# Kernel tuning notes

Measured on AMD Instinct MI355X. Metric: run time of the kernel, lower is better.

Reference implementation:

```python
import jax, jax.numpy as jnp
import numpy as np

ANCHORS_ALL = jnp.array([[10.,13.],[16.,30.],[33.,23.],[30.,61.],[62.,45.],
                         [59.,119.],[116.,90.],[156.,198.],[373.,326.]], dtype=jnp.float32)
INDICES = jnp.array([0, 1, 2], dtype=jnp.int32)   # anchor indices of level 0
ANCH_LVL = ANCHORS_ALL[0:3]                        # [nA, 2] anchors for this level
STRIDE = 8.0
N_CLS = 80
NA = 3


def _bce_logits(x, t):
    # elementwise binary_cross_entropy_with_logits (same formula as torch)
    return jnp.maximum(x, 0.0) - x * t + jnp.log1p(jnp.exp(-jnp.abs(x)))


def _iou_cxcywh(a, b):
    # a: [..., 4], b: [..., 4] (broadcastable), boxes as (cx, cy, w, h)
    ax1, ax2 = a[..., 0] - a[..., 2] * 0.5, a[..., 0] + a[..., 2] * 0.5
    ay1, ay2 = a[..., 1] - a[..., 3] * 0.5, a[..., 1] + a[..., 3] * 0.5
    bx1, bx2 = b[..., 0] - b[..., 2] * 0.5, b[..., 0] + b[..., 2] * 0.5
    by1, by2 = b[..., 1] - b[..., 3] * 0.5, b[..., 1] + b[..., 3] * 0.5
    iw = jnp.clip(jnp.minimum(ax2, bx2) - jnp.maximum(ax1, bx1), 0.0)
    ih = jnp.clip(jnp.minimum(ay2, by2) - jnp.maximum(ay1, by1), 0.0)
    inter = iw * ih
    union = (ax2 - ax1) * (ay2 - ay1) + (bx2 - bx1) * (by2 - by1) - inter
    return inter / (union + 1e-16)


def setup_inputs() -> dict:
    key = jax.random.key(0)
    ks = jax.random.split(key, 7)
    nB, nA, nH, nW, G = 8, 3, 160, 160, 32
    t_bbox = jax.random.normal(ks[0], (nB, nA, nH, nW, 4), jnp.float32)
    conf_logits = jax.random.normal(ks[1], (nB, nA, nH, nW, 1), jnp.float32)
    cls_logits = jax.random.normal(ks[2], (nB, nA, nH, nW, N_CLS), jnp.float32)
    cxy = jax.random.uniform(ks[3], (nB, G, 2), jnp.float32, 20.0, 1260.0)
    wh = jax.random.uniform(ks[4], (nB, G, 2), jnp.float32, 5.0, 60.0)
    gt_bboxes = jnp.concatenate([cxy, wh], axis=-1)           # cxcywh
    gt_cls = jax.random.randint(ks[5], (nB, G), 0, N_CLS, jnp.int32)
    gt_mask = jax.random.uniform(ks[6], (nB, G)) < 0.8        # padded-GT validity
    return dict(t_bbox=t_bbox, conf_logits=conf_logits, cls_logits=cls_logits,
                gt_bboxes=gt_bboxes, gt_cls=gt_cls, gt_mask=gt_mask)


def reference(t_bbox, conf_logits, cls_logits, gt_bboxes, gt_cls, gt_mask):
    nB, nA, nH, nW, _ = t_bbox.shape
    N = nA * nH * nW
    # ---- bbox decode (torch does this on a detached copy) ----
    sig = jax.nn.sigmoid(jax.lax.stop_gradient(t_bbox))
    yv, xv = jnp.meshgrid(jnp.arange(nH), jnp.arange(nW), indexing='ij')
    grid = jnp.stack([xv, yv], axis=-1).astype(jnp.float32).reshape(1, 1, nH, nW, 2)
    p_xy = (sig[..., 0:2] * 2.0 - 0.5 + grid) * STRIDE
    p_wh = (sig[..., 2:4] * 2.0) ** 2 * ANCH_LVL.reshape(1, nA, 1, 1, 2)
    p_bbox = jnp.concatenate([p_xy, p_wh], axis=-1).reshape(nB, N, 4)
    p_conf = jax.nn.sigmoid(jax.lax.stop_gradient(conf_logits))       # [nB,nA,nH,nW,1]
    p_cls = jax.nn.sigmoid(jax.lax.stop_gradient(cls_logits))
    cls_score = jnp.max(p_cls, axis=-1, keepdims=True)
    cls_idx = jnp.argmax(p_cls, axis=-1).reshape(nB, N)
    score = (p_conf * cls_score).reshape(nB, N)
    # ---- per-GT best-anchor matching (vectorized over [nB, G]) ----
    gw, gh = gt_bboxes[..., 2], gt_bboxes[..., 3]
    aw, ah = ANCHORS_ALL[:, 0], ANCHORS_ALL[:, 1]
    inter = jnp.minimum(gw[..., None], aw) * jnp.minimum(gh[..., None], ah)
    union = (gw * gh)[..., None] + aw * ah - inter
    anch_idx = jnp.argmax(inter / (union + 1e-16), axis=-1)           # [nB,G]
    matched = jnp.any(anch_idx[..., None] == INDICES, axis=-1)
    valid = gt_mask & matched
    ta = (anch_idx % NA).astype(jnp.int32)
    ti = jnp.clip((gt_bboxes[..., 0] / STRIDE).astype(jnp.int32), 0, nW - 1)
    tj = jnp.clip((gt_bboxes[..., 1] / STRIDE).astype(jnp.int32), 0, nH - 1)
    b_idx = jnp.arange(nB)[:, None]
    t_bb = t_bbox[b_idx, ta, tj, ti]       # [nB,G,4]
    t_cl = cls_logits[b_idx, ta, tj, ti]   # [nB,G,C]
    tgt_xy = ((gt_bboxes[..., 0:2] / STRIDE) % 1.0 + 0.5) / 2.0
    tgt_wh = jnp.sqrt(gt_bboxes[..., 2:4] / ANCH_LVL[ta]) / 2.0
    vm = valid.astype(t_bbox.dtype)
    loss_xy = jnp.sum(vm * jnp.sum(_bce_logits(t_bb[..., 0:2], tgt_xy), axis=-1))
    loss_wh = jnp.sum(vm * jnp.sum(_bce_logits(t_bb[..., 2:4], tgt_wh), axis=-1))
    onehot = jax.nn.one_hot(gt_cls, N_CLS, dtype=t_bbox.dtype)
    loss_cls = jnp.sum(vm * jnp.mean(_bce_logits(t_cl, onehot), axis=-1))
    # ---- objectness target: max IoU of every decoded box with the GTs ----
    ious = _iou_cxcywh(p_bbox[:, :, None, :], gt_bboxes[:, None, :, :])  # [nB,N,G]
    ious = jnp.where(gt_mask[:, None, :], ious, -1.0)
    has_gt = jnp.any(gt_mask, axis=-1)
    tconf = jnp.where(has_gt[:, None], jnp.max(ious, axis=-1), 0.0)
    tconf = tconf.reshape(nB, nA, nH, nW, 1)
    loss_conf = jnp.sum(_bce_logits(conf_logits, tconf))
    loss = (loss_xy + loss_wh + loss_conf + loss_cls) / nB
    return p_bbox, cls_idx, score, loss
```

## Files before the change

kernel.cpp:

```cpp
#include <hip/hip_runtime.h>

#define NB 8
#define NA 3
#define NH 160
#define NW 160
#define NCLS 80
#define NGT 32
#define NPB (NA * NH * NW)
#define TOTAL (NB * NPB)
#define NBLK (TOTAL / 256)
#define OFF_CLSIDX (TOTAL * 4)
#define OFF_SCORE  (TOTAL * 5)
#define OFF_LOSS   (TOTAL * 6)

#define F4_PER_ROW 20

__device__ float g_acc = 0.0f;

__device__ __forceinline__ float det_sigmoid(float x) { return 1.0f / (1.0f + expf(-x)); }
__device__ __forceinline__ float det_bce(float x, float t) {
    return fmaxf(x, 0.0f) - x * t + log1pf(expf(-fabsf(x)));
}
__device__ __forceinline__ float det_aw3(int a) { return a == 0 ? 10.0f : (a == 1 ? 16.0f : 33.0f); }
__device__ __forceinline__ float det_ah3(int a) { return a == 0 ? 13.0f : (a == 1 ? 30.0f : 23.0f); }

__device__ __forceinline__ bool det_mask_is_u8(const void* p) {
    const unsigned int* w = (const unsigned int*)p;
    unsigned int acc = 0;
#pragma unroll
    for (int k = 0; k < 64; k++) acc |= (w[k] & 0xFFFFFF00u);
    return acc != 0;
}
__device__ __forceinline__ bool det_mask_at(const void* p, bool u8mode, int idx) {
    return u8mode ? (((const unsigned char*)p)[idx] != 0)
                  : (((const int*)p)[idx] != 0);
}

__device__ __forceinline__ float det_gt_loss(int tid,
        const float* __restrict__ t_bbox,
        const float* __restrict__ cls_logits,
        const float* __restrict__ gt_bboxes,
        const int* __restrict__ gt_cls,
        const void* __restrict__ gt_mask) {
    bool u8mode = det_mask_is_u8(gt_mask);
    int b = tid >> 5;
    int g = tid & 31;
    float4 gtb = ((const float4*)gt_bboxes)[b * NGT + g];
    float cx = gtb.x, cy = gtb.y, gw = gtb.z, gh = gtb.w;

    const float aw9[9] = {10.f,16.f,33.f,30.f,62.f,59.f,116.f,156.f,373.f};
    const float ah9[9] = {13.f,30.f,23.f,61.f,45.f,119.f,90.f,198.f,326.f};
    float garea = gw * gh;
    int aidx = 0;
    float best = -1.0f;
#pragma unroll
    for (int k = 0; k < 9; k++) {
        float inter = fminf(gw, aw9[k]) * fminf(gh, ah9[k]);
        float uni = garea + aw9[k] * ah9[k] - inter;
        float r = inter / (uni + 1e-16f);
        if (r > best) { best = r; aidx = k; }
    }
    bool valid = det_mask_at(gt_mask, u8mode, b * NGT + g) && (aidx < NA);
    int ta = aidx % NA;
    int ti = min(max((int)(cx * 0.125f), 0), NW - 1);
    int tj = min(max((int)(cy * 0.125f), 0), NH - 1);
    size_t cell = ((size_t)(b * NA + ta) * NH + tj) * NW + ti;

    float4 tb = ((const float4*)t_bbox)[cell];
    float fx = cx * 0.125f; fx -= floorf(fx);
    float fy = cy * 0.125f; fy -= floorf(fy);
    float tx = (fx + 0.5f) * 0.5f;
    float ty = (fy + 0.5f) * 0.5f;
    float tw = sqrtf(gw / det_aw3(ta)) * 0.5f;
    float th = sqrtf(gh / det_ah3(ta)) * 0.5f;

    float l = det_bce(tb.x, tx) + det_bce(tb.y, ty) +
              det_bce(tb.z, tw) + det_bce(tb.w, th);

    const float4* cl = (const float4*)(cls_logits + cell * NCLS);
    int tc = gt_cls[b * NGT + g];
    float lc = 0.0f;
#pragma unroll
    for (int c4 = 0; c4 < NCLS / 4; c4++) {
        float4 v = cl[c4];
        int c = c4 * 4;
        lc += det_bce(v.x, (c + 0 == tc) ? 1.0f : 0.0f);
        lc += det_bce(v.y, (c + 1 == tc) ? 1.0f : 0.0f);
        lc += det_bce(v.z, (c + 2 == tc) ? 1.0f : 0.0f);
        lc += det_bce(v.w, (c + 3 == tc) ? 1.0f : 0.0f);
    }
    l += lc * (1.0f / NCLS);
    return valid ? l : 0.0f;
}

__device__ __forceinline__ void det_issue_tile(const float4* g4, float4* ldsbase,
                                               size_t f4base, int l) {
#pragma unroll
    for (int k = 0; k < 5; ++k) {
        __builtin_amdgcn_global_load_lds(
            (const __attribute__((address_space(1))) void*)(g4 + f4base + k * 64 + l),
            (__attribute__((address_space(3))) void*)(ldsbase + k * 64),
            16, 0, 0);
    }
}

#define DET_WAITVM0() do { \
    asm volatile("s_waitcnt vmcnt(0)" ::: "memory"); \
    __builtin_amdgcn_sched_barrier(0); \
} while (0)
#define DET_WAITLGKM0() do { \
    asm volatile("s_waitcnt lgkmcnt(0)" ::: "memory"); \
    __builtin_amdgcn_sched_barrier(0); \
} while (0)

__global__ __launch_bounds__(256, 7) void det_all_k(
    const float* __restrict__ t_bbox,
    const float* __restrict__ conf_logits,
    const float* __restrict__ cls_logits,
    const float* __restrict__ gt_bboxes,
    const int* __restrict__ gt_cls,
    const void* __restrict__ gt_mask,
    float* __restrict__ out) {
    __shared__ float4 s_cls[4][16 * F4_PER_ROW];
    __shared__ float4 s_box[NGT];
    __shared__ float2 s_am[NGT];
    __shared__ float s_part[4];

    int tid = threadIdx.x;
    int blockCell = blockIdx.x * 256;
    int gid = blockCell + tid;
    int b = gid / NPB;
    int r = gid % NPB;

    if (tid < NGT) {
        bool u8mode = det_mask_is_u8(gt_mask);
        float4 gtb = ((const float4*)gt_bboxes)[b * NGT + tid];
        float4 bx;
        bx.x = gtb.x - gtb.z * 0.5f;
        bx.y = gtb.y - gtb.w * 0.5f;
        bx.z = gtb.x + gtb.z * 0.5f;
        bx.w = gtb.y + gtb.w * 0.5f;
        s_box[tid] = bx;
        float2 am;
        am.x = gtb.z * gtb.w;
        am.y = det_mask_at(gt_mask, u8mode, b * NGT + tid) ? 1.0f : 0.0f;
        s_am[tid] = am;
    }
    __syncthreads();

    int a   = r / (NH * NW);
    int rem = r % (NH * NW);
    int j   = rem / NW;
    int i   = rem % NW;

    float4 tb = ((const float4*)t_bbox)[gid];
    float confl = conf_logits[gid];
    float s0 = det_sigmoid(tb.x), s1 = det_sigmoid(tb.y);
    float s2 = det_sigmoid(tb.z), s3 = det_sigmoid(tb.w);
    float px = (s0 * 2.0f - 0.5f + (float)i) * 8.0f;
    float py = (s1 * 2.0f - 0.5f + (float)j) * 8.0f;
    float sw = s2 * 2.0f, sh = s3 * 2.0f;
    float pw = sw * sw * det_aw3(a);
    float ph = sh * sh * det_ah3(a);
    float4 pb; pb.x = px; pb.y = py; pb.z = pw; pb.w = ph;
    ((float4*)out)[gid] = pb;

    int w = tid >> 6, l = tid & 63;
    int cl_ = l >> 2;
    int q   = l & 3;
    const float4* g4 = (const float4*)cls_logits;
    int wbase = blockCell + w * 64;
    float4* t0 = &s_cls[w][0];
    __builtin_amdgcn_sched_barrier(0);
    det_issue_tile(g4, t0, (size_t)wbase * F4_PER_ROW, l);
    __builtin_amdgcn_sched_barrier(0);

    float px1 = px - pw * 0.5f, px2 = px + pw * 0.5f;
    float py1 = py - ph * 0.5f, py2 = py + ph * 0.5f;
    float parea = pw * ph;
    float maxiou = 0.0f;
#pragma unroll
    for (int g = 0; g < NGT; g++) {
        float4 bx = s_box[g];
        float2 am = s_am[g];
        float iw = fmaxf(fminf(px2, bx.z) - fmaxf(px1, bx.x), 0.0f);
        float ih = fmaxf(fminf(py2, bx.w) - fmaxf(py1, bx.y), 0.0f);
        float inter = iw * ih;
        float uni = parea + am.x - inter;
        float iou = inter / (uni + 1e-16f);
        maxiou = fmaxf(maxiou, (am.y != 0.0f) ? iou : 0.0f);
    }

    float sconf = det_sigmoid(confl);
    float lconf = det_bce(confl, maxiou);

    if (blockIdx.x == 0)
        lconf += det_gt_loss(tid, t_bbox, cls_logits, gt_bboxes, gt_cls, gt_mask);

#pragma unroll
    for (int off = 32; off > 0; off >>= 1) lconf += __shfl_down(lconf, off, 64);
    if (l == 0) s_part[w] = lconf;

#pragma unroll
    for (int it = 0; it < 4; ++it) {
        DET_WAITVM0();
        const float4* rowp = t0 + cl_ * F4_PER_ROW + q * 5;
        float4 v0 = rowp[0];
        float4 v1 = rowp[1];
        float4 v2 = rowp[2];
        float4 v3 = rowp[3];
        float4 v4 = rowp[4];
        DET_WAITLGKM0();
        if (it < 3)
            det_issue_tile(g4, t0, (size_t)(wbase + (it + 1) * 16) * F4_PER_ROW, l);

        float mx = -1e30f;
        int mi = 0;
        int cb = q * 20;
        { int c = cb;
          if (v0.x > mx) { mx = v0.x; mi = c + 0; }
          if (v0.y > mx) { mx = v0.y; mi = c + 1; }
          if (v0.z > mx) { mx = v0.z; mi = c + 2; }
          if (v0.w > mx) { mx = v0.w; mi = c + 3; } }
        { int c = cb + 4;
          if (v1.x > mx) { mx = v1.x; mi = c + 0; }
          if (v1.y > mx) { mx = v1.y; mi = c + 1; }
          if (v1.z > mx) { mx = v1.z; mi = c + 2; }
          if (v1.w > mx) { mx = v1.w; mi = c + 3; } }
        { int c = cb + 8;
          if (v2.x > mx) { mx = v2.x; mi = c + 0; }
          if (v2.y > mx) { mx = v2.y; mi = c + 1; }
          if (v2.z > mx) { mx = v2.z; mi = c + 2; }
          if (v2.w > mx) { mx = v2.w; mi = c + 3; } }
        { int c = cb + 12;
          if (v3.x > mx) { mx = v3.x; mi = c + 0; }
          if (v3.y > mx) { mx = v3.y; mi = c + 1; }
          if (v3.z > mx) { mx = v3.z; mi = c + 2; }
          if (v3.w > mx) { mx = v3.w; mi = c + 3; } }
        { int c = cb + 16;
          if (v4.x > mx) { mx = v4.x; mi = c + 0; }
          if (v4.y > mx) { mx = v4.y; mi = c + 1; }
          if (v4.z > mx) { mx = v4.z; mi = c + 2; }
          if (v4.w > mx) { mx = v4.w; mi = c + 3; } }

#pragma unroll
        for (int s = 1; s < 4; s <<= 1) {
            float ov = __shfl_xor(mx, s, 64);
            int   oi = __shfl_xor(mi, s, 64);
            if (ov > mx || (ov == mx && oi < mi)) { mx = ov; mi = oi; }
        }
        float sc = __shfl(sconf, it * 16 + cl_, 64);
        if (q == 0) {
            int cellg = wbase + it * 16 + cl_;
            out[OFF_CLSIDX + cellg] = (float)mi;
            out[OFF_SCORE  + cellg] = sc * det_sigmoid(mx);
        }
    }

    __syncthreads();
    if (tid == 0)
        atomicAdd(&g_acc, s_part[0] + s_part[1] + s_part[2] + s_part[3]);
}

__global__ void det_fin_k(float* __restrict__ out) {
    out[OFF_LOSS] = g_acc * (1.0f / NB);
    g_acc = 0.0f;
}

extern "C" void kernel_launch(void* const* d_in, const int* in_sizes, int n_in,
                              void* d_out, int out_size, void* d_ws, size_t ws_size,
                              hipStream_t stream) {
    (void)in_sizes; (void)n_in; (void)out_size; (void)d_ws; (void)ws_size;
    const float* t_bbox      = (const float*)d_in[0];
    const float* conf_logits = (const float*)d_in[1];
    const float* cls_logits  = (const float*)d_in[2];
    const float* gt_bboxes   = (const float*)d_in[3];
    const int*   gt_cls      = (const int*)d_in[4];
    const void*  gt_mask     = (const void*)d_in[5];
    float* out = (float*)d_out;

    det_all_k<<<NBLK, 256, 0, stream>>>(t_bbox, conf_logits, cls_logits,
                                        gt_bboxes, gt_cls, gt_mask, out);
    det_fin_k<<<1, 1, 0, stream>>>(out);
}
```

Measured before the change: 309.9 us.

## Load class logits directly from global instead of async LDS staging

```diff
diff --git a/kernel.cpp b/kernel.cpp
--- a/kernel.cpp
+++ b/kernel.cpp
@@ -93,27 +93,7 @@
     return valid ? l : 0.0f;
 }
 
-__device__ __forceinline__ void det_issue_tile(const float4* g4, float4* ldsbase,
-                                               size_t f4base, int l) {
-#pragma unroll
-    for (int k = 0; k < 5; ++k) {
-        __builtin_amdgcn_global_load_lds(
-            (const __attribute__((address_space(1))) void*)(g4 + f4base + k * 64 + l),
-            (__attribute__((address_space(3))) void*)(ldsbase + k * 64),
-            16, 0, 0);
-    }
-}
-
-#define DET_WAITVM0() do { \
-    asm volatile("s_waitcnt vmcnt(0)" ::: "memory"); \
-    __builtin_amdgcn_sched_barrier(0); \
-} while (0)
-#define DET_WAITLGKM0() do { \
-    asm volatile("s_waitcnt lgkmcnt(0)" ::: "memory"); \
-    __builtin_amdgcn_sched_barrier(0); \
-} while (0)
-
-__global__ __launch_bounds__(256, 7) void det_all_k(
+__global__ __launch_bounds__(256, 6) void det_all_k(
     const float* __restrict__ t_bbox,
     const float* __restrict__ conf_logits,
     const float* __restrict__ cls_logits,
@@ -121,7 +101,6 @@
     const int* __restrict__ gt_cls,
     const void* __restrict__ gt_mask,
     float* __restrict__ out) {
-    __shared__ float4 s_cls[4][16 * F4_PER_ROW];
     __shared__ float4 s_box[NGT];
     __shared__ float2 s_am[NGT];
     __shared__ float s_part[4];
@@ -165,16 +144,6 @@
     float4 pb; pb.x = px; pb.y = py; pb.z = pw; pb.w = ph;
     ((float4*)out)[gid] = pb;
 
-    int w = tid >> 6, l = tid & 63;
-    int cl_ = l >> 2;
-    int q   = l & 3;
-    const float4* g4 = (const float4*)cls_logits;
-    int wbase = blockCell + w * 64;
-    float4* t0 = &s_cls[w][0];
-    __builtin_amdgcn_sched_barrier(0);
-    det_issue_tile(g4, t0, (size_t)wbase * F4_PER_ROW, l);
-    __builtin_amdgcn_sched_barrier(0);
-
     float px1 = px - pw * 0.5f, px2 = px + pw * 0.5f;
     float py1 = py - ph * 0.5f, py2 = py + ph * 0.5f;
     float parea = pw * ph;
@@ -199,20 +168,23 @@
 
 #pragma unroll
     for (int off = 32; off > 0; off >>= 1) lconf += __shfl_down(lconf, off, 64);
+    int w = tid >> 6, l = tid & 63;
     if (l == 0) s_part[w] = lconf;
 
+    int cl_ = l >> 2;
+    int q   = l & 3;
+    const float4* g4 = (const float4*)cls_logits;
+    int wbase = blockCell + w * 64;
+
 #pragma unroll
     for (int it = 0; it < 4; ++it) {
-        DET_WAITVM0();
-        const float4* rowp = t0 + cl_ * F4_PER_ROW + q * 5;
+        int tileCell = wbase + it * 16;
+        const float4* rowp = g4 + (size_t)(tileCell + cl_) * F4_PER_ROW + q * 5;
         float4 v0 = rowp[0];
         float4 v1 = rowp[1];
         float4 v2 = rowp[2];
         float4 v3 = rowp[3];
         float4 v4 = rowp[4];
-        DET_WAITLGKM0();
-        if (it < 3)
-            det_issue_tile(g4, t0, (size_t)(wbase + (it + 1) * 16) * F4_PER_ROW, l);
 
         float mx = -1e30f;
         int mi = 0;
@@ -251,7 +223,7 @@
         }
         float sc = __shfl(sconf, it * 16 + cl_, 64);
         if (q == 0) {
-            int cellg = wbase + it * 16 + cl_;
+            int cellg = tileCell + cl_;
             out[OFF_CLSIDX + cellg] = (float)mi;
             out[OFF_SCORE  + cellg] = sc * det_sigmoid(mx);
         }
```

Measured after the change: 323.5 us. 1.04x slower.

## Use single-wave blocks with double-buffered LDS class tiles and spread atomics

Applied to the files above, without the earlier changes.

```diff
diff --git a/kernel.cpp b/kernel.cpp
--- a/kernel.cpp
+++ b/kernel.cpp
@@ -8,16 +8,22 @@
 #define NGT 32
 #define NPB (NA * NH * NW)
 #define TOTAL (NB * NPB)
-#define NBLK (TOTAL / 256)
+#define BLK 64
+#define NBLK (TOTAL / BLK)
 #define OFF_CLSIDX (TOTAL * 4)
 #define OFF_SCORE  (TOTAL * 5)
 #define OFF_LOSS   (TOTAL * 6)
 
 #define F4_PER_ROW 20
 
-__device__ float g_acc = 0.0f;
-
-__device__ __forceinline__ float det_sigmoid(float x) { return 1.0f / (1.0f + expf(-x)); }
+__device__ float g_acc[8 * 16];
+
+__device__ __forceinline__ float det_rcp(float x) {
+    return __builtin_amdgcn_rcpf(x);
+}
+__device__ __forceinline__ float det_sigmoid(float x) {
+    return det_rcp(1.0f + expf(-x));
+}
 __device__ __forceinline__ float det_bce(float x, float t) {
     return fmaxf(x, 0.0f) - x * t + log1pf(expf(-fabsf(x)));
 }
@@ -104,16 +110,12 @@
     }
 }
 
-#define DET_WAITVM0() do { \
-    asm volatile("s_waitcnt vmcnt(0)" ::: "memory"); \
+#define DET_WAITVM(N) do { \
+    asm volatile("s_waitcnt vmcnt(" #N ")" ::: "memory"); \
     __builtin_amdgcn_sched_barrier(0); \
 } while (0)
-#define DET_WAITLGKM0() do { \
-    asm volatile("s_waitcnt lgkmcnt(0)" ::: "memory"); \
-    __builtin_amdgcn_sched_barrier(0); \
-} while (0)
-
-__global__ __launch_bounds__(256, 7) void det_all_k(
+
+__global__ __launch_bounds__(64, 4) void det_all_k(
     const float* __restrict__ t_bbox,
     const float* __restrict__ conf_logits,
     const float* __restrict__ cls_logits,
@@ -121,32 +123,30 @@
     const int* __restrict__ gt_cls,
     const void* __restrict__ gt_mask,
     float* __restrict__ out) {
-    __shared__ float4 s_cls[4][16 * F4_PER_ROW];
+    __shared__ float4 s_cls[2][16 * F4_PER_ROW];
     __shared__ float4 s_box[NGT];
     __shared__ float2 s_am[NGT];
-    __shared__ float s_part[4];
-
-    int tid = threadIdx.x;
-    int blockCell = blockIdx.x * 256;
-    int gid = blockCell + tid;
+
+    int l = threadIdx.x;
+    int blockCell = blockIdx.x * BLK;
+    int gid = blockCell + l;
     int b = gid / NPB;
     int r = gid % NPB;
 
-    if (tid < NGT) {
+    if (l < NGT) {
         bool u8mode = det_mask_is_u8(gt_mask);
-        float4 gtb = ((const float4*)gt_bboxes)[b * NGT + tid];
+        float4 gtb = ((const float4*)gt_bboxes)[b * NGT + l];
         float4 bx;
         bx.x = gtb.x - gtb.z * 0.5f;
         bx.y = gtb.y - gtb.w * 0.5f;
         bx.z = gtb.x + gtb.z * 0.5f;
         bx.w = gtb.y + gtb.w * 0.5f;
-        s_box[tid] = bx;
+        s_box[l] = bx;
         float2 am;
         am.x = gtb.z * gtb.w;
-        am.y = det_mask_at(gt_mask, u8mode, b * NGT + tid) ? 1.0f : 0.0f;
-        s_am[tid] = am;
-    }
-    __syncthreads();
+        am.y = det_mask_at(gt_mask, u8mode, b * NGT + l) ? 1.0f : 0.0f;
+        s_am[l] = am;
+    }
 
     int a   = r / (NH * NW);
     int rem = r % (NH * NW);
@@ -165,14 +165,14 @@
     float4 pb; pb.x = px; pb.y = py; pb.z = pw; pb.w = ph;
     ((float4*)out)[gid] = pb;
 
-    int w = tid >> 6, l = tid & 63;
     int cl_ = l >> 2;
     int q   = l & 3;
     const float4* g4 = (const float4*)cls_logits;
-    int wbase = blockCell + w * 64;
-    float4* t0 = &s_cls[w][0];
+    float4* t0 = &s_cls[0][0];
+    float4* t1 = &s_cls[1][0];
     __builtin_amdgcn_sched_barrier(0);
-    det_issue_tile(g4, t0, (size_t)wbase * F4_PER_ROW, l);
+    det_issue_tile(g4, t0, (size_t)(blockCell +  0) * F4_PER_ROW, l);
+    det_issue_tile(g4, t1, (size_t)(blockCell + 16) * F4_PER_ROW, l);
     __builtin_amdgcn_sched_barrier(0);
 
     float px1 = px - pw * 0.5f, px2 = px + pw * 0.5f;
@@ -187,32 +187,38 @@
         float ih = fmaxf(fminf(py2, bx.w) - fmaxf(py1, bx.y), 0.0f);
         float inter = iw * ih;
         float uni = parea + am.x - inter;
-        float iou = inter / (uni + 1e-16f);
+        float iou = inter * det_rcp(uni + 1e-16f);
         maxiou = fmaxf(maxiou, (am.y != 0.0f) ? iou : 0.0f);
     }
 
     float sconf = det_sigmoid(confl);
     float lconf = det_bce(confl, maxiou);
 
-    if (blockIdx.x == 0)
-        lconf += det_gt_loss(tid, t_bbox, cls_logits, gt_bboxes, gt_cls, gt_mask);
+    if (blockIdx.x < 4)
+        lconf += det_gt_loss(blockIdx.x * BLK + l,
+                             t_bbox, cls_logits, gt_bboxes, gt_cls, gt_mask);
 
 #pragma unroll
     for (int off = 32; off > 0; off >>= 1) lconf += __shfl_down(lconf, off, 64);
-    if (l == 0) s_part[w] = lconf;
 
 #pragma unroll
     for (int it = 0; it < 4; ++it) {
-        DET_WAITVM0();
-        const float4* rowp = t0 + cl_ * F4_PER_ROW + q * 5;
+        if (it < 3) DET_WAITVM(5);
+        else        DET_WAITVM(0);
+        const float4* tile = (it & 1) ? t1 : t0;
+        const float4* rowp = tile + cl_ * F4_PER_ROW + q * 5;
         float4 v0 = rowp[0];
         float4 v1 = rowp[1];
         float4 v2 = rowp[2];
         float4 v3 = rowp[3];
         float4 v4 = rowp[4];
-        DET_WAITLGKM0();
-        if (it < 3)
-            det_issue_tile(g4, t0, (size_t)(wbase + (it + 1) * 16) * F4_PER_ROW, l);
+        if (it < 2) {
+            __builtin_amdgcn_sched_barrier(0);
+            asm volatile("s_waitcnt lgkmcnt(0)" ::: "memory");
+            __builtin_amdgcn_sched_barrier(0);
+            det_issue_tile(g4, (float4*)tile,
+                           (size_t)(blockCell + (it + 2) * 16) * F4_PER_ROW, l);
+        }
 
         float mx = -1e30f;
         int mi = 0;
@@ -251,20 +257,21 @@
         }
         float sc = __shfl(sconf, it * 16 + cl_, 64);
         if (q == 0) {
-            int cellg = wbase + it * 16 + cl_;
+            int cellg = blockCell + it * 16 + cl_;
             out[OFF_CLSIDX + cellg] = (float)mi;
             out[OFF_SCORE  + cellg] = sc * det_sigmoid(mx);
         }
     }
 
-    __syncthreads();
-    if (tid == 0)
-        atomicAdd(&g_acc, s_part[0] + s_part[1] + s_part[2] + s_part[3]);
+    if (l == 0)
+        atomicAdd(&g_acc[(blockIdx.x & 7) * 16], lconf);
 }
 
 __global__ void det_fin_k(float* __restrict__ out) {
-    out[OFF_LOSS] = g_acc * (1.0f / NB);
-    g_acc = 0.0f;
+    float tot = 0.0f;
+#pragma unroll
+    for (int s = 0; s < 8; ++s) { tot += g_acc[s * 16]; g_acc[s * 16] = 0.0f; }
+    out[OFF_LOSS] = tot * (1.0f / NB);
 }
 
 extern "C" void kernel_launch(void* const* d_in, const int* in_sizes, int n_in,
@@ -279,7 +286,7 @@
     const void*  gt_mask     = (const void*)d_in[5];
     float* out = (float*)d_out;
 
-    det_all_k<<<NBLK, 256, 0, stream>>>(t_bbox, conf_logits, cls_logits,
+    det_all_k<<<NBLK, BLK, 0, stream>>>(t_bbox, conf_logits, cls_logits,
                                         gt_bboxes, gt_cls, gt_mask, out);
     det_fin_k<<<1, 1, 0, stream>>>(out);
 }
```

New measurement: 299.5 us. 3.4% less time.
